# Optimization experiments

Hardware: AMD Instinct MI355X
Metric: run time of the kernel (lower is better)

## Reference

```python
import jax, jax.numpy as jnp
import numpy as np

N, E, D, K, B = 50000, 600000, 128, 8, 64
E_DIM = 16  # edge_attr feature dim (hard-coded nn.Linear(16, in_dim))


def setup_inputs() -> dict:
    key = jax.random.key(0)
    ks = jax.random.split(key, 10)
    x = jax.random.normal(ks[0], (N, D), dtype=jnp.float32)
    edge_index = jax.random.randint(ks[1], (2, E), 0, N)
    edge_attr = jax.random.normal(ks[2], (E, E_DIM), dtype=jnp.float32)
    # binary pocket membership mask [N, K]
    pkt_mask = (jax.random.uniform(ks[3], (N, K)) < 0.3).astype(jnp.float32)
    batch = jnp.sort(jax.random.randint(ks[4], (N,), 0, B))
    s = 1.0 / np.sqrt(D)
    We = jax.random.normal(ks[5], (E_DIM, D), dtype=jnp.float32) * (1.0 / np.sqrt(E_DIM))
    be = jnp.zeros((D,), jnp.float32)
    W1 = jax.random.normal(ks[6], (D, D), dtype=jnp.float32) * s
    b1 = jnp.zeros((D,), jnp.float32)
    W2 = jax.random.normal(ks[7], (D, D), dtype=jnp.float32) * s
    b2 = jnp.zeros((D,), jnp.float32)
    eps = jnp.zeros((), jnp.float32)  # GINEConv train_eps init 0
    gamma = jnp.ones((D,), jnp.float32)
    beta = jnp.zeros((D,), jnp.float32)
    Wv = jax.random.normal(ks[8], (D, D), dtype=jnp.float32) * s
    bv = jnp.zeros((D,), jnp.float32)
    return {"x": x, "edge_index": edge_index, "edge_attr": edge_attr,
            "pkt_mask": pkt_mask, "batch": batch,
            "We": We, "be": be, "W1": W1, "b1": b1, "W2": W2, "b2": b2,
            "eps": eps, "gamma": gamma, "beta": beta, "Wv": Wv, "bv": bv}


def reference(x, edge_index, edge_attr, pkt_mask, batch,
              We, be, W1, b1, W2, b2, eps, gamma, beta, Wv, bv):
    src, dst = edge_index[0], edge_index[1]
    # edge_lin: [E,16] -> [E,D]
    edge_emb = edge_attr @ We + be
    # GINEConv: message = relu(x_src + edge_emb), scatter-add at dst
    msg = jax.nn.relu(x[src] + edge_emb)
    agg = jax.ops.segment_sum(msg, dst, num_segments=N)
    h = (1.0 + eps) * x + agg
    x_res = jax.nn.relu(h @ W1 + b1) @ W2 + b2  # nn MLP
    # virtual feedback: pocket-wise masked mean pooling per graph
    xw = x_res[:, None, :] * pkt_mask[:, :, None]          # [N,K,D]
    pocket_sum = jax.ops.segment_sum(xw.reshape(N, K * D), batch,
                                     num_segments=B).reshape(B, K, D)
    pocket_count = jax.ops.segment_sum(pkt_mask, batch, num_segments=B)  # [B,K]
    pocket_mean = pocket_sum / (pocket_count[:, :, None] + 1e-9)
    pocket_emb = pocket_mean @ Wv + bv                      # [B,K,D]
    node_pe = pocket_emb[batch]                             # gather -> [N,K,D]
    x_res = x_res + (node_pe * pkt_mask[:, :, None]).sum(axis=1)
    # LayerNorm (eps=1e-5, population variance as in torch)
    mu = x_res.mean(axis=-1, keepdims=True)
    var = ((x_res - mu) ** 2).mean(axis=-1, keepdims=True)
    y = (x_res - mu) / jnp.sqrt(var + 1e-5) * gamma + beta
    # ReLU activation; dropout is identity in eval mode
    return jax.nn.relu(y)
```

## Files before the change

kernel.cpp:

```cpp
#include <hip/hip_runtime.h>
#include <hip/hip_bf16.h>
#include <stdint.h>

#define D 128
#define K 8
#define BGRAPH 64
#define CH 64
#define GRP 4

typedef __attribute__((ext_vector_type(8))) short bf16x8;
typedef __attribute__((ext_vector_type(4))) float f32x4;
typedef __attribute__((ext_vector_type(2))) float f32x2;

__device__ __forceinline__ short f2bf(float f) {
    union { float f; uint32_t u; } v; v.f = f;
    const uint32_t r = (v.u + 0x7fffu + ((v.u >> 16) & 1u)) >> 16;
    return (short)r;
}
__device__ __forceinline__ float bflo(uint32_t u) {
    union { uint32_t u; float f; } v; v.u = u << 16; return v.f;
}
__device__ __forceinline__ float bfhi(uint32_t u) {
    union { uint32_t u; float f; } v; v.u = u & 0xffff0000u; return v.f;
}

__global__ __launch_bounds__(256) void prep_kernel(
    const float* __restrict__ x, const float* __restrict__ ea,
    const float* __restrict__ W1, const float* __restrict__ W2,
    const int* __restrict__ dst,
    __hip_bfloat16* __restrict__ xb, short* __restrict__ eab,
    short* __restrict__ wb1t, short* __restrict__ wb2t,
    int* __restrict__ deg,
    int NX, int NEA, int E, int NBX, int NBE, int NBW)
{
    const int b = blockIdx.x;
    const int t = threadIdx.x;
    if (b < NBX) {
        const int i = b * 2048 + t * 8;
        if (i + 8 <= NX) {
            const float4 a = *(const float4*)(x + i);
            const float4 c = *(const float4*)(x + i + 4);
            short v[8];
            v[0] = f2bf(a.x); v[1] = f2bf(a.y); v[2] = f2bf(a.z); v[3] = f2bf(a.w);
            v[4] = f2bf(c.x); v[5] = f2bf(c.y); v[6] = f2bf(c.z); v[7] = f2bf(c.w);
            *(uint4*)((short*)xb + i) = *(const uint4*)v;
        }
    } else if (b < NBX + NBE) {
        const int i = (b - NBX) * 2048 + t * 8;
        if (i + 8 <= NEA) {
            const float4 a = *(const float4*)(ea + i);
            const float4 c = *(const float4*)(ea + i + 4);
            short v[8];
            v[0] = f2bf(a.x); v[1] = f2bf(a.y); v[2] = f2bf(a.z); v[3] = f2bf(a.w);
            v[4] = f2bf(c.x); v[5] = f2bf(c.y); v[6] = f2bf(c.z); v[7] = f2bf(c.w);
            *(uint4*)(eab + i) = *(const uint4*)v;
        }
    } else if (b < NBX + NBE + NBW) {
        const int idx = (b - NBX - NBE) * 256 + t;
        const int which = idx >> 14;
        const int rem = idx & 16383;
        const int n = rem >> 7;
        const int k = rem & 127;
        const float* W = which ? W2 : W1;
        short* O = which ? wb2t : wb1t;
        O[n * D + k] = f2bf(W[(size_t)k * D + n]);
    } else {
        const int i = ((b - NBX - NBE - NBW) * 256 + t) * 4;
        if (i + 4 <= E) {
            const int4 v = *(const int4*)(dst + i);
            atomicAdd(&deg[v.x], 1);
            atomicAdd(&deg[v.y], 1);
            atomicAdd(&deg[v.z], 1);
            atomicAdd(&deg[v.w], 1);
        } else {
            for (int j = i; j < E; ++j) atomicAdd(&deg[dst[j]], 1);
        }
    }
}

__global__ __launch_bounds__(256) void scan_partial_kernel(
    const int* __restrict__ deg, int* __restrict__ bsum, int N)
{
    const int t = threadIdx.x;
    const int base = (blockIdx.x * 256 + t) * 4;
    int s = 0;
    if (base + 4 <= N) {
        const int4 v = *(const int4*)(deg + base);
        s = v.x + v.y + v.z + v.w;
    } else {
        for (int j = base; j < N; ++j) s += deg[j];
    }
    __shared__ int red[256];
    red[t] = s;
    __syncthreads();
    for (int off = 128; off; off >>= 1) {
        if (t < off) red[t] += red[t + off];
        __syncthreads();
    }
    if (t == 0) bsum[blockIdx.x] = red[0];
}

__global__ __launch_bounds__(64) void scan_top_kernel(
    const int* __restrict__ bsum, int* __restrict__ boffs, int nb)
{
    __shared__ int sh[64];
    const int t = threadIdx.x;
    const int v = (t < nb) ? bsum[t] : 0;
    sh[t] = v;
    __syncthreads();
    for (int off = 1; off < 64; off <<= 1) {
        const int u = (t >= off) ? sh[t - off] : 0;
        __syncthreads();
        sh[t] += u;
        __syncthreads();
    }
    if (t < nb) boffs[t] = sh[t] - v;
}

__global__ __launch_bounds__(256) void scan_final_kernel(
    const int* __restrict__ deg, const int* __restrict__ boffs,
    int* __restrict__ cursor, int N)
{
    const int t = threadIdx.x;
    const int base = (blockIdx.x * 256 + t) * 4;
    int v0 = 0, v1 = 0, v2 = 0, v3 = 0;
    if (base + 4 <= N) {
        const int4 v = *(const int4*)(deg + base);
        v0 = v.x; v1 = v.y; v2 = v.z; v3 = v.w;
    } else {
        if (base     < N) v0 = deg[base];
        if (base + 1 < N) v1 = deg[base + 1];
        if (base + 2 < N) v2 = deg[base + 2];
        if (base + 3 < N) v3 = deg[base + 3];
    }
    const int s = v0 + v1 + v2 + v3;
    __shared__ int sh[256];
    sh[t] = s;
    __syncthreads();
    for (int off = 1; off < 256; off <<= 1) {
        const int u = (t >= off) ? sh[t - off] : 0;
        __syncthreads();
        sh[t] += u;
        __syncthreads();
    }
    int ex = boffs[blockIdx.x] + sh[t] - s;
    if (base < N)     { cursor[base]     = ex; } ex += v0;
    if (base + 1 < N) { cursor[base + 1] = ex; } ex += v1;
    if (base + 2 < N) { cursor[base + 2] = ex; } ex += v2;
    if (base + 3 < N) { cursor[base + 3] = ex; }
}

__global__ __launch_bounds__(256) void scatter_kernel(
    const int* __restrict__ src, const int* __restrict__ dst,
    int* __restrict__ cursor, uint2* __restrict__ md, int E)
{
    const int i = blockIdx.x * 256 + threadIdx.x;
    if (i < E) {
        const unsigned sv = (unsigned)src[i];
        const unsigned dv = (unsigned)dst[i];
        const int p = atomicAdd(&cursor[dv], 1);
        md[p] = make_uint2(sv | (dv << 16), (unsigned)i);
    }
}

__device__ __forceinline__ void flush_row(
    float* __restrict__ agg, int node, int d, f32x2 acc, int first, int last)
{
    float* p = agg + (size_t)node * D + d;
    if (node == first || node == last) {
        if (acc.x != 0.f) atomicAdd(p,     acc.x);
        if (acc.y != 0.f) atomicAdd(p + 1, acc.y);
    } else {
        *(f32x2*)p = acc;
    }
}

__global__ __launch_bounds__(256) void gine_reduce_kernel(
    const __hip_bfloat16* __restrict__ xb, const uint2* __restrict__ md,
    const short* __restrict__ eab, const float* __restrict__ We,
    const float* __restrict__ be, float* __restrict__ agg, int E)
{
    const int wave = threadIdx.x >> 6;
    const int lane = threadIdx.x & 63;
    const int chunk = __builtin_amdgcn_readfirstlane(blockIdx.x * 4 + wave);
    const int e0 = chunk * CH;
    if (e0 >= E) return;
    const int d = lane * 2;
    const int NG = CH / GRP;

    f32x2 w[16];
    #pragma unroll
    for (int j = 0; j < 16; ++j) w[j] = *(const f32x2*)(We + j * D + d);
    const f32x2 bb = *(const f32x2*)(be + d);

    uint2 ma[GRP], mb[GRP], mc[GRP];
    #pragma unroll
    for (int j = 0; j < GRP; ++j) ma[j] = md[e0 + j];
    #pragma unroll
    for (int j = 0; j < GRP; ++j) mb[j] = md[e0 + GRP + j];
    #pragma unroll
    for (int j = 0; j < GRP; ++j) mc[j] = md[e0 + 2 * GRP + j];

    uint4 ea0[GRP][2];
    #pragma unroll
    for (int j = 0; j < GRP; ++j) {
        const uint4* p = (const uint4*)(eab + (size_t)ma[j].y * 16);
        ea0[j][0] = p[0]; ea0[j][1] = p[1];
    }
    uint32_t xcur[GRP], xn1[GRP];
    #pragma unroll
    for (int j = 0; j < GRP; ++j)
        xcur[j] = *(const uint32_t*)(xb + (size_t)(ma[j].x & 0xffffu) * D + d);
    #pragma unroll
    for (int j = 0; j < GRP; ++j)
        xn1[j] = *(const uint32_t*)(xb + (size_t)(mb[j].x & 0xffffu) * D + d);

    const int first = (int)(ma[0].x >> 16);
    const int last  = (int)(md[e0 + CH - 1].x >> 16);

    f32x2 acc = {0.f, 0.f};
    int cur = first;

    for (int g = 0; g < NG; ++g) {
        uint2 mnew[GRP] = {};
        uint4 ean[GRP][2] = {};
        uint32_t xn2[GRP] = {};
        if (g + 3 < NG) {
            #pragma unroll
            for (int j = 0; j < GRP; ++j) mnew[j] = md[e0 + (g + 3) * GRP + j];
        }
        if (g + 1 < NG) {
            #pragma unroll
            for (int j = 0; j < GRP; ++j) {
                const uint4* p = (const uint4*)(eab + (size_t)mb[j].y * 16);
                ean[j][0] = p[0]; ean[j][1] = p[1];
            }
        }
        if (g + 2 < NG) {
            #pragma unroll
            for (int j = 0; j < GRP; ++j)
                xn2[j] = *(const uint32_t*)(xb + (size_t)(mc[j].x & 0xffffu) * D + d);
        }

        #pragma unroll
        for (int j = 0; j < GRP; ++j) {
            const int dk = (int)(ma[j].x >> 16);
            if (dk != cur) {
                flush_row(agg, cur, d, acc, first, last);
                acc.x = 0.f; acc.y = 0.f;
                cur = dk;
            }
            const uint32_t xu = xcur[j];
            f32x2 m;
            m.x = bb.x + bflo(xu);
            m.y = bb.y + bfhi(xu);
            const uint4 ua = ea0[j][0];
            const uint4 ub = ea0[j][1];
            const uint32_t ud[8] = {ua.x, ua.y, ua.z, ua.w,
                                    ub.x, ub.y, ub.z, ub.w};
            #pragma unroll
            for (int t = 0; t < 8; ++t) {
                const float a0 = bflo(ud[t]);
                const float a1 = bfhi(ud[t]);
                const f32x2 av0 = {a0, a0};
                const f32x2 av1 = {a1, a1};
                m += av0 * w[2 * t];
                m += av1 * w[2 * t + 1];
            }
            f32x2 r;
            r.x = m.x > 0.f ? m.x : 0.f;
            r.y = m.y > 0.f ? m.y : 0.f;
            acc += r;
        }

        #pragma unroll
        for (int j = 0; j < GRP; ++j) {
            ma[j] = mb[j]; mb[j] = mc[j]; mc[j] = mnew[j];
            ea0[j][0] = ean[j][0]; ea0[j][1] = ean[j][1];
            xcur[j] = xn1[j]; xn1[j] = xn2[j];
        }
    }
    flush_row(agg, cur, d, acc, first, last);
}

#define MROWS 64
#define HSTR  132
__global__ __launch_bounds__(256) void mlp_mfma_kernel(
    const float* __restrict__ x, const float* __restrict__ agg,
    const float* __restrict__ epsp,
    const short* __restrict__ wb1t, const float* __restrict__ b1,
    const short* __restrict__ wb2t, const float* __restrict__ b2,
    float* __restrict__ xres, int N)
{
    __shared__ float hsh[MROWS * HSTR];
    const int row0 = blockIdx.x * MROWS;
    const float ep = 1.0f + epsp[0];

    for (int i = threadIdx.x; i < MROWS * D / 4; i += 256) {
        const int flat = i * 4;
        const int r = flat >> 7;
        const int c = flat & (D - 1);
        const int row = row0 + r;
        float4 hv = make_float4(0.f, 0.f, 0.f, 0.f);
        if (row < N) {
            const float4 xv = *(const float4*)(x   + (size_t)row * D + c);
            const float4 av = *(const float4*)(agg + (size_t)row * D + c);
            hv = make_float4(ep * xv.x + av.x, ep * xv.y + av.y,
                             ep * xv.z + av.z, ep * xv.w + av.w);
        }
        *(float4*)(hsh + r * HSTR + c) = hv;
    }
    __syncthreads();

    const int lane = threadIdx.x & 63;
    const int wrow = (threadIdx.x >> 6) * 16;
    const int m = lane & 15;
    const int q = lane >> 4;

    f32x4 acc[8];

    #pragma unroll
    for (int ct = 0; ct < 8; ++ct) {
        const float b = b1[ct * 16 + m];
        acc[ct] = (f32x4){b, b, b, b};
    }
    #pragma unroll
    for (int ks = 0; ks < 4; ++ks) {
        const float* ap = hsh + (wrow + m) * HSTR + ks * 32 + q * 8;
        float av[8];
        *(float4*)(av)     = *(const float4*)ap;
        *(float4*)(av + 4) = *(const float4*)(ap + 4);
        bf16x8 a;
        #pragma unroll
        for (int j = 0; j < 8; ++j) a[j] = f2bf(av[j]);
        #pragma unroll
        for (int ct = 0; ct < 8; ++ct) {
            const bf16x8 b = *(const bf16x8*)(wb1t + (ct * 16 + m) * D + ks * 32 + q * 8);
            acc[ct] = __builtin_amdgcn_mfma_f32_16x16x32_bf16(a, b, acc[ct], 0, 0, 0);
        }
    }
    #pragma unroll
    for (int ct = 0; ct < 8; ++ct)
        #pragma unroll
        for (int r = 0; r < 4; ++r) {
            const float v = acc[ct][r];
            hsh[(wrow + q * 4 + r) * HSTR + ct * 16 + m] = v > 0.f ? v : 0.f;
        }

    #pragma unroll
    for (int ct = 0; ct < 8; ++ct) {
        const float b = b2[ct * 16 + m];
        acc[ct] = (f32x4){b, b, b, b};
    }
    #pragma unroll
    for (int ks = 0; ks < 4; ++ks) {
        const float* ap = hsh + (wrow + m) * HSTR + ks * 32 + q * 8;
        float av[8];
        *(float4*)(av)     = *(const float4*)ap;
        *(float4*)(av + 4) = *(const float4*)(ap + 4);
        bf16x8 a;
        #pragma unroll
        for (int j = 0; j < 8; ++j) a[j] = f2bf(av[j]);
        #pragma unroll
        for (int ct = 0; ct < 8; ++ct) {
            const bf16x8 b = *(const bf16x8*)(wb2t + (ct * 16 + m) * D + ks * 32 + q * 8);
            acc[ct] = __builtin_amdgcn_mfma_f32_16x16x32_bf16(a, b, acc[ct], 0, 0, 0);
        }
    }
    #pragma unroll
    for (int r = 0; r < 4; ++r) {
        const int row = row0 + wrow + q * 4 + r;
        if (row < N) {
            #pragma unroll
            for (int ct = 0; ct < 8; ++ct)
                xres[(size_t)row * D + ct * 16 + m] = acc[ct][r];
        }
    }
}

#define PPARTS 32
__global__ __launch_bounds__(128) void pocket_sum_kernel(
    const float* __restrict__ xres, const float* __restrict__ pmask,
    const int* __restrict__ batch,
    float* __restrict__ psum, float* __restrict__ pcnt, int N)
{
    const int g = blockIdx.x / PPARTS;
    const int part = blockIdx.x % PPARTS;

    int lo, hi;
    {
        int l = 0, r = N;
        while (l < r) { int m = (l + r) >> 1; if (batch[m] < g) l = m + 1; else r = m; }
        lo = l;
        r = N;
        while (l < r) { int m = (l + r) >> 1; if (batch[m] < g + 1) l = m + 1; else r = m; }
        hi = l;
    }
    const int cnt = hi - lo;
    const int per = (cnt + PPARTS - 1) / PPARTS;
    const int s = lo + part * per;
    const int e = min(s + per, hi);

    const int d = threadIdx.x;
    float acc[K];
    #pragma unroll
    for (int k = 0; k < K; ++k) acc[k] = 0.0f;
    float c = 0.0f;

    for (int n = s; n < e; ++n) {
        const float xv = xres[(size_t)n * D + d];
        const float4 m0 = *(const float4*)(pmask + (size_t)n * K);
        const float4 m1 = *(const float4*)(pmask + (size_t)n * K + 4);
        acc[0] += m0.x * xv; acc[1] += m0.y * xv;
        acc[2] += m0.z * xv; acc[3] += m0.w * xv;
        acc[4] += m1.x * xv; acc[5] += m1.y * xv;
        acc[6] += m1.z * xv; acc[7] += m1.w * xv;
        if (d < K) c += pmask[(size_t)n * K + d];
    }
    #pragma unroll
    for (int k = 0; k < K; ++k)
        atomicAdd(&psum[(size_t)g * (K * D) + k * D + d], acc[k]);
    if (d < K) atomicAdd(&pcnt[g * K + d], c);
}

__global__ __launch_bounds__(128) void pocket_emb_kernel(
    const float* __restrict__ psum, const float* __restrict__ pcnt,
    const float* __restrict__ Wv, const float* __restrict__ bv,
    float* __restrict__ pemb)
{
    __shared__ float smean[K * D];
    __shared__ float scnt[K];
    const int g = blockIdx.x;
    const int d = threadIdx.x;
    if (d < K) scnt[d] = pcnt[g * K + d];
    __syncthreads();
    #pragma unroll
    for (int k = 0; k < K; ++k)
        smean[k * D + d] = psum[(size_t)g * (K * D) + k * D + d] / (scnt[k] + 1e-9f);
    __syncthreads();

    float acc[K];
    const float bvv = bv[d];
    #pragma unroll
    for (int k = 0; k < K; ++k) acc[k] = bvv;
    for (int j = 0; j < D; ++j) {
        const float w = Wv[j * D + d];
        #pragma unroll
        for (int k = 0; k < K; ++k) acc[k] += smean[k * D + j] * w;
    }
    #pragma unroll
    for (int k = 0; k < K; ++k)
        pemb[(size_t)g * (K * D) + k * D + d] = acc[k];
}

__global__ __launch_bounds__(256) void ln_kernel(
    const float* __restrict__ xres, const float* __restrict__ pmask,
    const int* __restrict__ batch, const float* __restrict__ pemb,
    const float* __restrict__ gamma, const float* __restrict__ beta,
    float* __restrict__ out, int N)
{
    const int wave = threadIdx.x >> 6;
    const int lane = threadIdx.x & 63;
    const int n = blockIdx.x * 4 + wave;
    if (n >= N) return;
    const int d = lane * 2;

    float2 v = *(const float2*)(xres + (size_t)n * D + d);
    const int g = batch[n];
    const float* pe = pemb + (size_t)g * (K * D);
    const float4 m0 = *(const float4*)(pmask + (size_t)n * K);
    const float4 m1 = *(const float4*)(pmask + (size_t)n * K + 4);
    const float mk[K] = {m0.x, m0.y, m0.z, m0.w, m1.x, m1.y, m1.z, m1.w};
    #pragma unroll
    for (int k = 0; k < K; ++k) {
        if (mk[k] != 0.0f) {
            const float2 p = *(const float2*)(pe + k * D + d);
            v.x += mk[k] * p.x;
            v.y += mk[k] * p.y;
        }
    }

    float s = v.x + v.y;
    #pragma unroll
    for (int off = 32; off; off >>= 1) s += __shfl_xor(s, off, 64);
    const float mu = s * (1.0f / 128.0f);
    const float d0 = v.x - mu, d1 = v.y - mu;
    float sq = d0 * d0 + d1 * d1;
    #pragma unroll
    for (int off = 32; off; off >>= 1) sq += __shfl_xor(sq, off, 64);
    const float var = sq * (1.0f / 128.0f);
    const float inv = rsqrtf(var + 1e-5f);

    const float2 gm = *(const float2*)(gamma + d);
    const float2 bt = *(const float2*)(beta + d);
    float y0 = d0 * inv * gm.x + bt.x;
    float y1 = d1 * inv * gm.y + bt.y;
    y0 = y0 > 0.0f ? y0 : 0.0f;
    y1 = y1 > 0.0f ? y1 : 0.0f;
    *(float2*)(out + (size_t)n * D + d) = make_float2(y0, y1);
}

extern "C" void kernel_launch(void* const* d_in, const int* in_sizes, int n_in,
                              void* d_out, int out_size, void* d_ws, size_t ws_size,
                              hipStream_t stream)
{
    const float* x     = (const float*)d_in[0];
    const int*   ei    = (const int*)  d_in[1];
    const float* ea    = (const float*)d_in[2];
    const float* pmask = (const float*)d_in[3];
    const int*   batch = (const int*)  d_in[4];
    const float* We    = (const float*)d_in[5];
    const float* be    = (const float*)d_in[6];
    const float* W1    = (const float*)d_in[7];
    const float* b1    = (const float*)d_in[8];
    const float* W2    = (const float*)d_in[9];
    const float* b2    = (const float*)d_in[10];
    const float* epsp  = (const float*)d_in[11];
    const float* gamma = (const float*)d_in[12];
    const float* beta  = (const float*)d_in[13];
    const float* Wv    = (const float*)d_in[14];
    const float* bv    = (const float*)d_in[15];
    float* out = (float*)d_out;

    const int N = in_sizes[0] / D;
    const int E = in_sizes[1] / 2;
    const int* src = ei;
    const int* dst = ei + E;

    int*   deg  = (int*)d_ws;
    float* agg  = (float*)(deg + N);
    float* psum = agg + (size_t)N * D;
    float* pcnt = psum + (size_t)BGRAPH * K * D;
    float* xres = pcnt + (size_t)BGRAPH * K;
    float* pemb = xres + (size_t)N * D;
    float* extra = pemb + (size_t)BGRAPH * K * D;
    __hip_bfloat16* xb = (__hip_bfloat16*)(extra + 128);
    short* wb1t = (short*)(xb + (size_t)N * D);
    short* wb2t = wb1t + (size_t)D * D;

    int*   cursor = (int*)xres;
    uint2* md  = (uint2*)(((uintptr_t)(cursor + N) + 15) & ~(uintptr_t)15);
    short* eab = (short*)(md + E);

    int*  bsum  = (int*)extra;
    int*  boffs = bsum + 64;

    const int nb = (N + 1023) / 1024;
    const int nchunks = (E + CH - 1) / CH;
    const int NX = N * D, NEA = E * 16;
    const int NBX = NX / 2048;
    const int NBE = (NEA / 8 + 255) / 256;
    const int NBW = (2 * D * D) / 256;
    const int NBH = (E / 4 + 255) / 256;

    const size_t zero_bytes =
        ((size_t)N + (size_t)N * D + (size_t)BGRAPH * K * D + BGRAPH * K) * sizeof(float);
    hipMemsetAsync(d_ws, 0, zero_bytes, stream);

    prep_kernel<<<NBX + NBE + NBW + NBH, 256, 0, stream>>>(
        x, ea, W1, W2, dst, xb, eab, wb1t, wb2t, deg, NX, NEA, E, NBX, NBE, NBW);
    scan_partial_kernel<<<nb, 256, 0, stream>>>(deg, bsum, N);
    scan_top_kernel<<<1, 64, 0, stream>>>(bsum, boffs, nb);
    scan_final_kernel<<<nb, 256, 0, stream>>>(deg, boffs, cursor, N);
    scatter_kernel<<<(E + 255) / 256, 256, 0, stream>>>(src, dst, cursor, md, E);
    gine_reduce_kernel<<<(nchunks + 3) / 4, 256, 0, stream>>>(
        xb, md, eab, We, be, agg, E);

    mlp_mfma_kernel<<<(N + MROWS - 1) / MROWS, 256, 0, stream>>>(
        x, agg, epsp, wb1t, b1, wb2t, b2, xres, N);
    pocket_sum_kernel<<<BGRAPH * PPARTS, 128, 0, stream>>>(
        xres, pmask, batch, psum, pcnt, N);
    pocket_emb_kernel<<<BGRAPH, 128, 0, stream>>>(psum, pcnt, Wv, bv, pemb);
    ln_kernel<<<(N + 3) / 4, 256, 0, stream>>>(
        xres, pmask, batch, pemb, gamma, beta, out, N);
}
```

Baseline: 376.8 us.

## Compute edge embeddings with bf16 MFMA using hi/lo split weights

```diff
diff --git a/kernel.cpp b/kernel.cpp
--- a/kernel.cpp
+++ b/kernel.cpp
@@ -27,9 +27,11 @@
 __global__ __launch_bounds__(256) void prep_kernel(
     const float* __restrict__ x, const float* __restrict__ ea,
     const float* __restrict__ W1, const float* __restrict__ W2,
+    const float* __restrict__ We, const float* __restrict__ be,
     const int* __restrict__ dst,
     __hip_bfloat16* __restrict__ xb, short* __restrict__ eab,
     short* __restrict__ wb1t, short* __restrict__ wb2t,
+    short* __restrict__ webt,
     int* __restrict__ deg,
     int NX, int NEA, int E, int NBX, int NBE, int NBW)
 {
@@ -57,13 +59,32 @@
         }
     } else if (b < NBX + NBE + NBW) {
         const int idx = (b - NBX - NBE) * 256 + t;
-        const int which = idx >> 14;
-        const int rem = idx & 16383;
-        const int n = rem >> 7;
-        const int k = rem & 127;
-        const float* W = which ? W2 : W1;
-        short* O = which ? wb2t : wb1t;
-        O[n * D + k] = f2bf(W[(size_t)k * D + n]);
+        if (idx < 2 * D * D) {
+            const int which = idx >> 14;
+            const int rem = idx & 16383;
+            const int n = rem >> 7;
+            const int k = rem & 127;
+            const float* W = which ? W2 : W1;
+            short* O = which ? wb2t : wb1t;
+            O[n * D + k] = f2bf(W[(size_t)k * D + n]);
+        } else {
+            const int widx = idx - 2 * D * D;
+            const int h = widx >> 12;
+            const int c = (widx >> 5) & 127;
+            const int k = widx & 31;
+            float val = 0.f;
+            if (k < 16) val = We[k * D + c];
+            else if (k == 16) val = be[c];
+            const short hi = f2bf(val);
+            short outv;
+            if (h == 0) outv = hi;
+            else {
+                union { uint32_t u; float f; } fh;
+                fh.u = ((uint32_t)(unsigned short)hi) << 16;
+                outv = f2bf(val - fh.f);
+            }
+            webt[(h << 12) + c * 32 + k] = outv;
+        }
     } else {
         const int i = ((b - NBX - NBE - NBW) * 256 + t) * 4;
         if (i + 4 <= E) {
@@ -177,21 +198,31 @@
 
 __global__ __launch_bounds__(256) void gine_reduce_kernel(
     const __hip_bfloat16* __restrict__ xb, const uint2* __restrict__ md,
-    const short* __restrict__ eab, const float* __restrict__ We,
-    const float* __restrict__ be, float* __restrict__ agg, int E)
-{
+    const short* __restrict__ eab, const short* __restrict__ webt,
+    float* __restrict__ agg, int E)
+{
+    __shared__ float lsh[4][16 * 132];
     const int wave = threadIdx.x >> 6;
     const int lane = threadIdx.x & 63;
     const int chunk = __builtin_amdgcn_readfirstlane(blockIdx.x * 4 + wave);
     const int e0 = chunk * CH;
     if (e0 >= E) return;
     const int d = lane * 2;
+    const int m = lane & 15;
+    const int q = lane >> 4;
+    float* myl = lsh[wave];
     const int NG = CH / GRP;
-
-    f32x2 w[16];
-    #pragma unroll
-    for (int j = 0; j < 16; ++j) w[j] = *(const f32x2*)(We + j * D + d);
-    const f32x2 bb = *(const f32x2*)(be + d);
+    const unsigned* mdu = (const unsigned*)md;
+
+    bf16x8 bH[8], bL[8];
+    #pragma unroll
+    for (int ct = 0; ct < 8; ++ct) {
+        bH[ct] = *(const bf16x8*)(webt +        (ct * 16 + m) * 32 + q * 8);
+        bL[ct] = *(const bf16x8*)(webt + 4096 + (ct * 16 + m) * 32 + q * 8);
+    }
+
+    uint4 afcur = *(const uint4*)(eab +
+        (size_t)mdu[2 * (e0 + m) + 1] * 16 + (q & 1) * 8);
 
     uint2 ma[GRP], mb[GRP], mc[GRP];
     #pragma unroll
@@ -201,12 +232,6 @@
     #pragma unroll
     for (int j = 0; j < GRP; ++j) mc[j] = md[e0 + 2 * GRP + j];
 
-    uint4 ea0[GRP][2];
-    #pragma unroll
-    for (int j = 0; j < GRP; ++j) {
-        const uint4* p = (const uint4*)(eab + (size_t)ma[j].y * 16);
-        ea0[j][0] = p[0]; ea0[j][1] = p[1];
-    }
     uint32_t xcur[GRP], xn1[GRP];
     #pragma unroll
     for (int j = 0; j < GRP; ++j)
@@ -222,19 +247,39 @@
     int cur = first;
 
     for (int g = 0; g < NG; ++g) {
+        if ((g & 3) == 0) {
+            const int mg = g >> 2;
+            uint4 afn = make_uint4(0u, 0u, 0u, 0u);
+            if (mg < 3)
+                afn = *(const uint4*)(eab +
+                    (size_t)mdu[2 * (e0 + (mg + 1) * 16 + m) + 1] * 16 +
+                    (q & 1) * 8);
+            uint4 au = afcur;
+            if (q >= 2)
+                au = make_uint4(q == 2 ? 0x3f80u : 0u, 0u, 0u, 0u);
+            const bf16x8 a = *(const bf16x8*)&au;
+            f32x4 mm[8];
+            #pragma unroll
+            for (int ct = 0; ct < 8; ++ct) {
+                const f32x4 z = {0.f, 0.f, 0.f, 0.f};
+                mm[ct] = __builtin_amdgcn_mfma_f32_16x16x32_bf16(a, bL[ct], z, 0, 0, 0);
+            }
+            #pragma unroll
+            for (int ct = 0; ct < 8; ++ct)
+                mm[ct] = __builtin_amdgcn_mfma_f32_16x16x32_bf16(a, bH[ct], mm[ct], 0, 0, 0);
+            #pragma unroll
+            for (int ct = 0; ct < 8; ++ct)
+                #pragma unroll
+                for (int r = 0; r < 4; ++r)
+                    myl[(q * 4 + r) * 132 + ct * 16 + m] = mm[ct][r];
+            afcur = afn;
+        }
+
         uint2 mnew[GRP] = {};
-        uint4 ean[GRP][2] = {};
         uint32_t xn2[GRP] = {};
         if (g + 3 < NG) {
             #pragma unroll
             for (int j = 0; j < GRP; ++j) mnew[j] = md[e0 + (g + 3) * GRP + j];
-        }
-        if (g + 1 < NG) {
-            #pragma unroll
-            for (int j = 0; j < GRP; ++j) {
-                const uint4* p = (const uint4*)(eab + (size_t)mb[j].y * 16);
-                ean[j][0] = p[0]; ean[j][1] = p[1];
-            }
         }
         if (g + 2 < NG) {
             #pragma unroll
@@ -251,32 +296,16 @@
                 cur = dk;
             }
             const uint32_t xu = xcur[j];
-            f32x2 m;
-            m.x = bb.x + bflo(xu);
-            m.y = bb.y + bfhi(xu);
-            const uint4 ua = ea0[j][0];
-            const uint4 ub = ea0[j][1];
-            const uint32_t ud[8] = {ua.x, ua.y, ua.z, ua.w,
-                                    ub.x, ub.y, ub.z, ub.w};
-            #pragma unroll
-            for (int t = 0; t < 8; ++t) {
-                const float a0 = bflo(ud[t]);
-                const float a1 = bfhi(ud[t]);
-                const f32x2 av0 = {a0, a0};
-                const f32x2 av1 = {a1, a1};
-                m += av0 * w[2 * t];
-                m += av1 * w[2 * t + 1];
-            }
-            f32x2 r;
-            r.x = m.x > 0.f ? m.x : 0.f;
-            r.y = m.y > 0.f ? m.y : 0.f;
-            acc += r;
+            const float2 em = *(const float2*)(myl + ((g & 3) * GRP + j) * 132 + d);
+            const float m0 = em.x + bflo(xu);
+            const float m1 = em.y + bfhi(xu);
+            acc.x += m0 > 0.f ? m0 : 0.f;
+            acc.y += m1 > 0.f ? m1 : 0.f;
         }
 
         #pragma unroll
         for (int j = 0; j < GRP; ++j) {
             ma[j] = mb[j]; mb[j] = mc[j]; mc[j] = mnew[j];
-            ea0[j][0] = ean[j][0]; ea0[j][1] = ean[j][1];
             xcur[j] = xn1[j]; xn1[j] = xn2[j];
         }
     }
@@ -537,6 +566,7 @@
     __hip_bfloat16* xb = (__hip_bfloat16*)(extra + 128);
     short* wb1t = (short*)(xb + (size_t)N * D);
     short* wb2t = wb1t + (size_t)D * D;
+    short* webt = wb2t + (size_t)D * D;
 
     int*   cursor = (int*)xres;
     uint2* md  = (uint2*)(((uintptr_t)(cursor + N) + 15) & ~(uintptr_t)15);
@@ -550,7 +580,7 @@
     const int NX = N * D, NEA = E * 16;
     const int NBX = NX / 2048;
     const int NBE = (NEA / 8 + 255) / 256;
-    const int NBW = (2 * D * D) / 256;
+    const int NBW = (2 * D * D + 2 * 128 * 32) / 256;
     const int NBH = (E / 4 + 255) / 256;
 
     const size_t zero_bytes =
@@ -558,13 +588,14 @@
     hipMemsetAsync(d_ws, 0, zero_bytes, stream);
 
     prep_kernel<<<NBX + NBE + NBW + NBH, 256, 0, stream>>>(
-        x, ea, W1, W2, dst, xb, eab, wb1t, wb2t, deg, NX, NEA, E, NBX, NBE, NBW);
+        x, ea, W1, W2, We, be, dst, xb, eab, wb1t, wb2t, webt, deg,
+        NX, NEA, E, NBX, NBE, NBW);
     scan_partial_kernel<<<nb, 256, 0, stream>>>(deg, bsum, N);
     scan_top_kernel<<<1, 64, 0, stream>>>(bsum, boffs, nb);
     scan_final_kernel<<<nb, 256, 0, stream>>>(deg, boffs, cursor, N);
     scatter_kernel<<<(E + 255) / 256, 256, 0, stream>>>(src, dst, cursor, md, E);
     gine_reduce_kernel<<<(nchunks + 3) / 4, 256, 0, stream>>>(
-        xb, md, eab, We, be, agg, E);
+        xb, md, eab, webt, agg, E);
 
     mlp_mfma_kernel<<<(N + MROWS - 1) / MROWS, 256, 0, stream>>>(
         x, agg, epsp, wb1t, b1, wb2t, b2, xres, N);
```

After: 359.3 us. -4.6%, faster.
